# Performance work log

Hardware: AMD Instinct MI355X
Metric: run time of the kernel (lower is better)

Reference implementation:

```python
import jax, jax.numpy as jnp
import numpy as np

B, N, E = 8, 64, 192
D_IN, D_PROJ = 1024, 256
F = 16            # cfg.NGM.GNN_FEAT per layer
SK_TAU = 0.05     # cfg.NGM.SK_TAU
SK_ITERS = 10
BIN_ITERS = 10
NN = N * N


def _project(x, Wp, bp, gamma, beta):
    # self.projection: Linear(1024,256) -> BatchNorm1d(256) (batch stats) -> ReLU
    B_, M, _ = x.shape
    h = x.reshape(B_ * M, -1) @ Wp + bp
    mu = h.mean(0)
    var = h.var(0)
    h = (h - mu) / jnp.sqrt(var + 1e-5) * gamma + beta
    return jax.nn.relu(h).reshape(B_, M, -1)


def _l2n(x):
    return x / jnp.clip(jnp.linalg.norm(x, axis=-1, keepdims=True), 1e-12)


def _log_sinkhorn(log_s, iters):
    for _ in range(iters):
        log_s = log_s - jax.nn.logsumexp(log_s, axis=2, keepdims=True)
        log_s = log_s - jax.nn.logsumexp(log_s, axis=1, keepdims=True)
    return jnp.exp(log_s)


def _build_K(Ke, Kp, s1, d1, s2, d2):
    # construct_sparse_aff_mat: K[a2*N+a1, b2*N+b1] += Ke[e1, e2]
    rows = s2[None, :] * N + s1[:, None]      # [E, E]
    cols = d2[None, :] * N + d1[:, None]      # [E, E]
    flat = (rows.astype(jnp.int32) * NN + cols.astype(jnp.int32)).ravel()
    K = jnp.zeros((NN * NN,), Ke.dtype).at[flat].add(Ke.ravel()).reshape(NN, NN)
    diag = jnp.arange(NN)
    # diagonal holds vec(Kp^T) (ordering a2*N + a1, matching emb = Kp.T.reshape(-1,1))
    return K.at[diag, diag].set(Kp.T.ravel())


def setup_inputs() -> dict:
    key = jax.random.key(0)
    ks = jax.random.split(key, 32)
    inp = {}
    inp['x1'] = jax.random.normal(ks[0], (B, N, D_IN), jnp.float32)
    inp['x2'] = jax.random.normal(ks[1], (B, N, D_IN), jnp.float32)
    inp['e1'] = jax.random.normal(ks[2], (B, E, D_IN), jnp.float32)
    inp['e2'] = jax.random.normal(ks[3], (B, E, D_IN), jnp.float32)
    inp['Wp'] = jax.random.normal(ks[4], (D_IN, D_PROJ), jnp.float32) * 0.02
    inp['bp'] = jnp.zeros((D_PROJ,), jnp.float32)
    inp['gamma'] = jnp.ones((D_PROJ,), jnp.float32)
    inp['beta'] = jnp.zeros((D_PROJ,), jnp.float32)
    in_dims = [1, F + 1, F + 1]
    for i, din in enumerate(in_dims):
        inp[f'W{i}'] = jax.random.normal(ks[5 + 3 * i], (din, F), jnp.float32) * 0.2
        inp[f'b{i}'] = jnp.zeros((F,), jnp.float32)
        inp[f'S{i}'] = jax.random.normal(ks[6 + 3 * i], (F, 1), jnp.float32) * 0.2
        inp[f'c{i}'] = jnp.zeros((1,), jnp.float32)
    inp['Wc'] = jax.random.normal(ks[20], (F + 1, 1), jnp.float32) * 0.2
    inp['bc'] = jnp.zeros((1,), jnp.float32)
    inp['bin_value'] = jnp.ones((1,), jnp.float32) * 0.2
    inp['src1'] = jax.random.randint(ks[21], (B, E), 0, N, jnp.int32)
    inp['dst1'] = jax.random.randint(ks[22], (B, E), 0, N, jnp.int32)
    inp['src2'] = jax.random.randint(ks[23], (B, E), 0, N, jnp.int32)
    inp['dst2'] = jax.random.randint(ks[24], (B, E), 0, N, jnp.int32)
    return inp


def reference(x1, x2, e1, e2, Wp, bp, gamma, beta,
              W0, b0, S0, c0, W1, b1, S1, c1, W2, b2, S2, c2,
              Wc, bc, bin_value, src1, dst1, src2, dst2):
    # unary / quadratic affinities via projected, L2-normalized inner products
    p1 = _project(x1, Wp, bp, gamma, beta)
    p2 = _project(x2, Wp, bp, gamma, beta)
    q1 = _project(e1, Wp, bp, gamma, beta)
    q2 = _project(e2, Wp, bp, gamma, beta)
    Kp = jnp.einsum('bnd,bmd->bnm', _l2n(p1), _l2n(p2))        # [B, N1, N2]
    Ke = 0.5 * jnp.einsum('bed,bfd->bef', _l2n(q1), _l2n(q2))  # [B, E1, E2]
    # sparse Kronecker affinity assembled densely (association graph adjacency)
    K = jax.vmap(_build_K)(Ke, Kp, src1, dst1, src2, dst2)     # [B, NN, NN]
    A = (K > 0).astype(K.dtype)
    deg = jnp.clip(A.sum(-1), 1.0)                              # [B, NN]
    x = Kp.transpose(0, 2, 1).reshape(B, NN, 1)                 # emb = vec(Kp^T)
    for (W, b, S, c) in ((W0, b0, S0, c0), (W1, b1, S1, c1), (W2, b2, S2, c2)):
        msg = jnp.einsum('bij,bjc->bic', K, x) / deg[..., None]  # sparse matvec (memory-bound)
        h = jax.nn.relu(msg @ W + b)                             # [B, NN, F]
        v = (h @ S + c).reshape(B, N, N)                         # row order a2*N+a1 -> [B, N2, N1]
        ss = _log_sinkhorn(v.transpose(0, 2, 1) / SK_TAU, SK_ITERS)  # Sinkhorn embedding channel
        x = jnp.concatenate([h, ss.transpose(0, 2, 1).reshape(B, NN, 1)], -1)
    v = (x @ Wc + bc).reshape(B, N, N)
    s = v.transpose(0, 2, 1)                                    # [B, N1, N2]
    # BinSinkhorn: pad with learned bin value, dual normalization, strip bin
    binv = bin_value[0]
    ls = jnp.concatenate([s, jnp.full((B, 1, N), binv, s.dtype)], 1)
    ls = jnp.concatenate([ls, jnp.full((B, N + 1, 1), binv, s.dtype)], 2)
    P = _log_sinkhorn(ls, BIN_ITERS)
    ss = P[:, :N, :N]
    return ss / jax.lax.stop_gradient(ss.max())
```

## Files before the change

### kernel.cpp

```cpp
#include <hip/hip_runtime.h>

constexpr int kB   = 8;
constexpr int kN   = 64;
constexpr int kE   = 192;
constexpr int kDin = 1024;
constexpr int kDp  = 256;
constexpr int kNN  = 4096;
constexpr float kTauInv = 20.0f;
constexpr int kXS  = 16;
constexpr int kXP  = 18;

typedef float vfloat4 __attribute__((ext_vector_type(4)));

struct SmemGemm {
    float As[2][16][68]; float Ws[2][16][68];
    float colS[64], colS2[64];
};
struct SmemCsr  {
    int km1[4096], km2[4096];
    short es1[kE], es2[kE], rp1[kE], rp2[kE];
    int cnt1[64], cnt2[64], pos1[64], pos2[64];
    int ccnt1[kE], ccnt2[kE], cpos1[kE], cpos2[kE];
};
union __align__(16) SmemK1 { SmemGemm g; SmemCsr csr; };

__global__ __launch_bounds__(256) void k_projcsr(
    const float* __restrict__ x1, const float* __restrict__ x2,
    const float* __restrict__ e1, const float* __restrict__ e2,
    const float* __restrict__ Wp, const float* __restrict__ bp,
    const int* __restrict__ src1, const int* __restrict__ dst1,
    const int* __restrict__ src2, const int* __restrict__ dst2,
    float* __restrict__ hbuf, float* __restrict__ stats,
    int* __restrict__ off1, int* __restrict__ off2,
    int* __restrict__ lst1, int* __restrict__ lst2,
    int* __restrict__ rep1g, int* __restrict__ rep2g,
    int* __restrict__ coff1, int* __restrict__ coff2,
    int* __restrict__ clst1, int* __restrict__ clst2)
{
    const int bid = blockIdx.x, t = threadIdx.x;
    __shared__ SmemK1 u;

    if (bid < 256) {
        const int rt = bid >> 2, ct = bid & 3;
        const int grow0 = rt * 64, col0 = ct * 64;
        const int seg = (rt < 8) ? 0 : (rt < 16 ? 1 : (rt < 40 ? 2 : 3));
        const float* src; int lrow0;
        if (rt < 8)       { src = x1; lrow0 = grow0; }
        else if (rt < 16) { src = x2; lrow0 = grow0 - 512; }
        else if (rt < 40) { src = e1; lrow0 = grow0 - 1024; }
        else              { src = e2; lrow0 = grow0 - 2560; }

        const int tx = t & 15, ty = t >> 4;
        const int arow = t >> 2, acol = (t & 3) * 4;
        const int wrow = t >> 4, wcol = (t & 15) * 4;
        if (t < 64) { u.g.colS[t] = 0.f; u.g.colS2[t] = 0.f; }

        const float* Abase = src + (size_t)(lrow0 + arow) * kDin + acol;
        const float* Wbase = Wp + (size_t)wrow * kDp + col0 + wcol;

        float4 a4 = *(const float4*)Abase;
        float4 w4 = *(const float4*)Wbase;
        float acc[4][4] = {};

        for (int c = 0; c < 64; ++c) {
            const int cur = c & 1;
            u.g.As[cur][acol + 0][arow] = a4.x;
            u.g.As[cur][acol + 1][arow] = a4.y;
            u.g.As[cur][acol + 2][arow] = a4.z;
            u.g.As[cur][acol + 3][arow] = a4.w;
            *(float4*)&u.g.Ws[cur][wrow][wcol] = w4;
            __syncthreads();
            if (c < 63) {
                a4 = *(const float4*)(Abase + (c + 1) * 16);
                w4 = *(const float4*)(Wbase + (size_t)(c + 1) * 16 * kDp);
            }
#pragma unroll
            for (int kk = 0; kk < 16; ++kk) {
                float4 av = *(const float4*)&u.g.As[cur][kk][ty * 4];
                float4 wv = *(const float4*)&u.g.Ws[cur][kk][tx * 4];
                float a[4] = {av.x, av.y, av.z, av.w};
                float w[4] = {wv.x, wv.y, wv.z, wv.w};
#pragma unroll
                for (int i = 0; i < 4; ++i)
#pragma unroll
                    for (int j = 0; j < 4; ++j)
                        acc[i][j] += a[i] * w[j];
            }
        }
        const float4 bb4 = *(const float4*)&bp[col0 + tx * 4];
        float sC[4] = {0.f, 0.f, 0.f, 0.f}, qC[4] = {0.f, 0.f, 0.f, 0.f};
#pragma unroll
        for (int i = 0; i < 4; ++i) {
            const int row = grow0 + ty * 4 + i;
            vfloat4 v;
            v.x = acc[i][0] + bb4.x; v.y = acc[i][1] + bb4.y;
            v.z = acc[i][2] + bb4.z; v.w = acc[i][3] + bb4.w;
            __builtin_nontemporal_store(v, (vfloat4*)&hbuf[(size_t)row * kDp + col0 + tx * 4]);
            sC[0] += v.x; sC[1] += v.y; sC[2] += v.z; sC[3] += v.w;
            qC[0] += v.x * v.x; qC[1] += v.y * v.y;
            qC[2] += v.z * v.z; qC[3] += v.w * v.w;
        }
#pragma unroll
        for (int j = 0; j < 4; ++j) {
            atomicAdd(&u.g.colS[tx * 4 + j], sC[j]);
            atomicAdd(&u.g.colS2[tx * 4 + j], qC[j]);
        }
        __syncthreads();
        if (t < 64) {
            atomicAdd(&stats[seg * 512 + col0 + t], u.g.colS[t]);
            atomicAdd(&stats[seg * 512 + 256 + col0 + t], u.g.colS2[t]);
        }
    } else {
        const int b = bid - 256;
        auto& C = u.csr;
        for (int i = t; i < 4096; i += 256) {
            C.km1[i] = 0x7fffffff; C.km2[i] = 0x7fffffff;
        }
        if (t < 64) { C.cnt1[t] = 0; C.cnt2[t] = 0; }
        for (int i = t; i < kE; i += 256) { C.ccnt1[i] = 0; C.ccnt2[i] = 0; }
        __syncthreads();
        if (t < kE) {
            int v1 = src1[b * kE + t], v2 = src2[b * kE + t];
            C.es1[t] = (short)v1; C.es2[t] = (short)v2;
            atomicAdd(&C.cnt1[v1], 1);
            atomicAdd(&C.cnt2[v2], 1);
            atomicMin(&C.km1[v1 * 64 + dst1[b * kE + t]], t);
            atomicMin(&C.km2[v2 * 64 + dst2[b * kE + t]], t);
        }
        __syncthreads();
        if (t < kE) {
            int r1 = C.km1[C.es1[t] * 64 + dst1[b * kE + t]];
            int r2 = C.km2[C.es2[t] * 64 + dst2[b * kE + t]];
            C.rp1[t] = (short)r1; C.rp2[t] = (short)r2;
            rep1g[b * kE + t] = r1; rep2g[b * kE + t] = r2;
            atomicAdd(&C.ccnt1[r1], 1);
            atomicAdd(&C.ccnt2[r2], 1);
        }
        __syncthreads();
        if (t == 0) {
            int a = 0, c = 0;
            for (int v = 0; v < 64; ++v) { C.pos1[v] = a; a += C.cnt1[v]; C.pos2[v] = c; c += C.cnt2[v]; }
            a = 0; c = 0;
            for (int v = 0; v < kE; ++v) { C.cpos1[v] = a; a += C.ccnt1[v]; C.cpos2[v] = c; c += C.ccnt2[v]; }
        }
        __syncthreads();
        if (t < 64) { off1[b * 65 + t] = C.pos1[t]; off2[b * 65 + t] = C.pos2[t]; }
        if (t == 0) { off1[b * 65 + 64] = kE; off2[b * 65 + 64] = kE; }
        if (t < kE) { coff1[b * 193 + t] = C.cpos1[t]; coff2[b * 193 + t] = C.cpos2[t]; }
        if (t == 0) { coff1[b * 193 + kE] = kE; coff2[b * 193 + kE] = kE; }
        __syncthreads();
        if (t < kE) {
            int p = atomicAdd(&C.pos1[C.es1[t]], 1); lst1[b * kE + p] = t;
            int q = atomicAdd(&C.pos2[C.es2[t]], 1); lst2[b * kE + q] = t;
            int cp = atomicAdd(&C.cpos1[C.rp1[t]], 1); clst1[b * kE + cp] = t;
            int cq = atomicAdd(&C.cpos2[C.rp2[t]], 1); clst2[b * kE + cq] = t;
        }
    }
}

struct __align__(16) SmemSim  {
    float Xs[32][36]; float Ys[32][36];
    float muX[256], isX[256], muY[256], isY[256];
    float ga[256], be[256];
    float scX[32], scY[32];
};

__global__ __launch_bounds__(256) void k_sim(
    const float* __restrict__ hbuf, const float* __restrict__ stats,
    const float* __restrict__ gamma, const float* __restrict__ beta,
    float* __restrict__ Kp, float* __restrict__ Ke)
{
    const int bid = blockIdx.x, t = threadIdx.x;
    __shared__ SmemSim u;

    const int id = bid % 40, b = bid / 40;
    int mt, nt_, ldo, segX, segY, xrow0, yrow0; float* outp; float scale;
    if (id < 4) {
        mt = (id >> 1) * 32; nt_ = (id & 1) * 32; ldo = 64;
        xrow0 = b * 64; yrow0 = 512 + b * 64;
        segX = 0; segY = 1;
        outp = Kp + (size_t)b * 4096; scale = 1.0f;
    } else {
        int e = id - 4;
        mt = (e / 6) * 32; nt_ = (e % 6) * 32; ldo = 192;
        xrow0 = 1024 + b * 192; yrow0 = 2560 + b * 192;
        segX = 2; segY = 3;
        outp = Ke + (size_t)b * 36864; scale = 0.5f;
    }
    {
        const float n = (segX < 2) ? 512.f : 1536.f;
        float mu = stats[segX * 512 + t] / n;
        float var = stats[segX * 512 + 256 + t] / n - mu * mu;
        u.muX[t] = mu; u.isX[t] = rsqrtf(var + 1e-5f);
        mu = stats[segY * 512 + t] / n;
        var = stats[segY * 512 + 256 + t] / n - mu * mu;
        u.muY[t] = mu; u.isY[t] = rsqrtf(var + 1e-5f);
        u.ga[t] = gamma[t]; u.be[t] = beta[t];
    }
    __syncthreads();
    {
        const int ri = t >> 2, lane = t & 3;
        const bool isXr = ri < 32;
        const int grow = isXr ? (xrow0 + mt + ri) : (yrow0 + nt_ + (ri - 32));
        const float* mus = isXr ? u.muX : u.muY;
        const float* iss = isXr ? u.isX : u.isY;
        const float* hr = hbuf + (size_t)grow * kDp;
        float ss = 0.f;
        for (int c4 = 0; c4 < 16; ++c4) {
            int c = lane * 64 + c4 * 4;
            float4 v = *(const float4*)&hr[c];
            float p;
            p = fmaxf((v.x - mus[c+0]) * iss[c+0] * u.ga[c+0] + u.be[c+0], 0.f); ss += p * p;
            p = fmaxf((v.y - mus[c+1]) * iss[c+1] * u.ga[c+1] + u.be[c+1], 0.f); ss += p * p;
            p = fmaxf((v.z - mus[c+2]) * iss[c+2] * u.ga[c+2] + u.be[c+2], 0.f); ss += p * p;
            p = fmaxf((v.w - mus[c+3]) * iss[c+3] * u.ga[c+3] + u.be[c+3], 0.f); ss += p * p;
        }
        ss += __shfl_xor(ss, 1);
        ss += __shfl_xor(ss, 2);
        if (lane == 0) {
            float sc = 1.f / fmaxf(sqrtf(ss), 1e-12f);
            if (isXr) u.scX[ri] = sc; else u.scY[ri - 32] = sc;
        }
    }
    __syncthreads();
    const int row = t >> 3, kq = t & 7;
    const int ty = t >> 4, tx = t & 15;
    const float* Xp = hbuf + (size_t)(xrow0 + mt) * kDp;
    const float* Yp = hbuf + (size_t)(yrow0 + nt_) * kDp;
    float acc[2][2] = {};
    for (int k0 = 0; k0 < kDp; k0 += 32) {
        const int c = k0 + kq * 4;
        float4 xa = *(const float4*)(Xp + (size_t)row * kDp + c);
        float4 ya = *(const float4*)(Yp + (size_t)row * kDp + c);
        const float sx = u.scX[row], sy = u.scY[row];
        u.Xs[kq*4+0][row] = fmaxf((xa.x - u.muX[c+0]) * u.isX[c+0] * u.ga[c+0] + u.be[c+0], 0.f) * sx;
        u.Xs[kq*4+1][row] = fmaxf((xa.y - u.muX[c+1]) * u.isX[c+1] * u.ga[c+1] + u.be[c+1], 0.f) * sx;
        u.Xs[kq*4+2][row] = fmaxf((xa.z - u.muX[c+2]) * u.isX[c+2] * u.ga[c+2] + u.be[c+2], 0.f) * sx;
        u.Xs[kq*4+3][row] = fmaxf((xa.w - u.muX[c+3]) * u.isX[c+3] * u.ga[c+3] + u.be[c+3], 0.f) * sx;
        u.Ys[kq*4+0][row] = fmaxf((ya.x - u.muY[c+0]) * u.isY[c+0] * u.ga[c+0] + u.be[c+0], 0.f) * sy;
        u.Ys[kq*4+1][row] = fmaxf((ya.y - u.muY[c+1]) * u.isY[c+1] * u.ga[c+1] + u.be[c+1], 0.f) * sy;
        u.Ys[kq*4+2][row] = fmaxf((ya.z - u.muY[c+2]) * u.isY[c+2] * u.ga[c+2] + u.be[c+2], 0.f) * sy;
        u.Ys[kq*4+3][row] = fmaxf((ya.w - u.muY[c+3]) * u.isY[c+3] * u.ga[c+3] + u.be[c+3], 0.f) * sy;
        __syncthreads();
#pragma unroll
        for (int kk = 0; kk < 32; ++kk) {
            float2 xv = *(const float2*)&u.Xs[kk][ty * 2];
            float2 yv = *(const float2*)&u.Ys[kk][tx * 2];
            acc[0][0] += xv.x * yv.x; acc[0][1] += xv.x * yv.y;
            acc[1][0] += xv.y * yv.x; acc[1][1] += xv.y * yv.y;
        }
        __syncthreads();
    }
#pragma unroll
    for (int i = 0; i < 2; ++i)
#pragma unroll
        for (int j = 0; j < 2; ++j)
            __builtin_nontemporal_store(scale * acc[i][j],
                &outp[(size_t)(mt + ty * 2 + i) * ldo + nt_ + tx * 2 + j]);
}

struct __align__(16) SmemLayer {
    float mat[64][68]; float fL[64], gL[64];
    float WL[17 * 16]; float bL[16], SL[16]; float c0v;
    float WcL[17];
    int jd2[kE]; int il[kE]; float msgT[64][18];
    int co1L[kE + 1], co2L[kE + 1];
    short cl1L[kE], cl2L[kE];
    float xs[64][kXP];
};

__device__ void sink64_local(int b, int t, float (*mat)[68], float* fL, float* gL,
                             const float* __restrict__ vin)
{
    const float4* v4 = (const float4*)(vin + b * kNN);
    for (int i = t; i < 1024; i += 256) {
        float4 v = v4[i];
        int idx = i * 4;
        int q = idx >> 6, p = idx & 63;
        mat[p][q]     = v.x * kTauInv;
        mat[p + 1][q] = v.y * kTauInv;
        mat[p + 2][q] = v.z * kTauInv;
        mat[p + 3][q] = v.w * kTauInv;
    }
    if (t < 64) { fL[t] = 0.f; gL[t] = 0.f; }
    __syncthreads();
    const int r = t >> 2, s = t & 3;
    float tv[16];
    for (int it = 0; it < 10; ++it) {
        float mx = -1e30f;
#pragma unroll
        for (int k = 0; k < 16; ++k) {
            float v = mat[r][s + 4 * k] + gL[s + 4 * k];
            tv[k] = v; mx = fmaxf(mx, v);
        }
        mx = fmaxf(mx, __shfl_xor(mx, 1));
        mx = fmaxf(mx, __shfl_xor(mx, 2));
        float sum = 0.f;
#pragma unroll
        for (int k = 0; k < 16; ++k) sum += __expf(tv[k] - mx);
        sum += __shfl_xor(sum, 1);
        sum += __shfl_xor(sum, 2);
        if (s == 0) fL[r] = -(mx + __logf(sum));
        __syncthreads();
        mx = -1e30f;
#pragma unroll
        for (int k = 0; k < 16; ++k) {
            float v = mat[s + 4 * k][r] + fL[s + 4 * k];
            tv[k] = v; mx = fmaxf(mx, v);
        }
        mx = fmaxf(mx, __shfl_xor(mx, 1));
        mx = fmaxf(mx, __shfl_xor(mx, 2));
        sum = 0.f;
#pragma unroll
        for (int k = 0; k < 16; ++k) sum += __expf(tv[k] - mx);
        sum += __shfl_xor(sum, 1);
        sum += __shfl_xor(sum, 2);
        if (s == 0) gL[r] = -(mx + __logf(sum));
        __syncthreads();
    }
    const float fr = fL[r];
#pragma unroll
    for (int k = 0; k < 16; ++k) {
        int q = s + 4 * k;
        mat[r][q] = __expf(mat[r][q] + fr + gL[q]);
    }
    __syncthreads();
}

template <int C, bool LASTP>
__device__ void layer_body(int bid, int t, SmemLayer& L,
    const int* __restrict__ off1, const int* __restrict__ lst1,
    const int* __restrict__ off2, const int* __restrict__ lst2,
    const int* __restrict__ d1, const int* __restrict__ d2,
    const int* __restrict__ rep1g, const int* __restrict__ rep2g,
    const int* __restrict__ coff1, const int* __restrict__ coff2,
    const int* __restrict__ clst1, const int* __restrict__ clst2,
    const float* __restrict__ Ke, const float* __restrict__ x,
    const float* __restrict__ Kp, int* __restrict__ degcnt,
    const float* __restrict__ W, const float* __restrict__ bb,
    const float* __restrict__ S, const float* __restrict__ c0,
    const float* __restrict__ Wc,
    const float* __restrict__ vprev, float* __restrict__ xn,
    float* __restrict__ vcbuf, float* __restrict__ vout)
{
    const int r2 = bid & 63, b = bid >> 6;
    for (int k = t; k < C * 16; k += 256) L.WL[k] = W[k];
    if (t < 16) { L.bL[t] = bb[t]; L.SL[t] = S[t]; }
    if (t == 0) L.c0v = c0[0];
    if (LASTP && t < 17) L.WcL[t] = Wc[t];
    const int j0 = off2[b * 65 + r2];
    const int n2 = off2[b * 65 + r2 + 1] - j0;
    for (int k = t; k < n2; k += 256) {
        int j = lst2[b * kE + j0 + k];
        int v = (j << 8) | d2[b * kE + j];
        if (C == 1 && rep2g[b * kE + j] == j) v |= 1 << 16;
        L.jd2[k] = v;
    }
    for (int k = t; k < kE; k += 256) {
        int i = lst1[b * kE + k];
        int v = (i << 8) | d1[b * kE + i];
        if (C == 1 && rep1g[b * kE + i] == i) v |= 1 << 16;
        L.il[k] = v;
    }
    if constexpr (C == 1) {
        for (int k = t; k < kE + 1; k += 256) {
            L.co1L[k] = coff1[b * 193 + k];
            L.co2L[k] = coff2[b * 193 + k];
        }
        for (int k = t; k < kE; k += 256) {
            L.cl1L[k] = (short)clst1[b * kE + k];
            L.cl2L[k] = (short)clst2[b * kE + k];
        }
    }
    if constexpr (C == 17) {
        sink64_local(b, t, L.mat, L.fL, L.gL, vprev);
    } else {
        __syncthreads();
    }

    const int r1 = t >> 2, lane = t & 3;
    const int i0 = off1[b * 65 + r1], i1 = off1[b * 65 + r1 + 1];
    const float* Keb = Ke + (size_t)b * kE * kE;
    const float* KpB = Kp + (size_t)b * kNN;
    int degLocal = 0;

    if constexpr (C == 1) {
        float acc = 0.f;
        for (int k = 0; k < n2; ++k) {
            int pk = L.jd2[k], j = (pk >> 8) & 255, dd2 = pk & 255;
            for (int m = i0 + lane; m < i1; m += 4) {
                int pi = L.il[m], i = (pi >> 8) & 255, dd1 = pi & 255;
                if (dd2 == r2 && dd1 == r1) continue;
                acc += Keb[(size_t)i * kE + j] * KpB[dd1 * 64 + dd2];
            }
        }
        acc += __shfl_xor(acc, 1);
        acc += __shfl_xor(acc, 2);
        if (lane == 0) L.msgT[r1][0] = acc;
        for (int m = i0 + lane; m < i1; m += 4) {
            int pi = L.il[m];
            if (!(pi >> 16)) continue;
            int i = (pi >> 8) & 255, dd1 = pi & 255;
            for (int k = 0; k < n2; ++k) {
                int pk = L.jd2[k];
                if (!(pk >> 16)) continue;
                int j = (pk >> 8) & 255, dd2 = pk & 255;
                float sum = 0.f;
                for (int mm = L.co1L[i]; mm < L.co1L[i + 1]; ++mm) {
                    const float* kr = Keb + (size_t)L.cl1L[mm] * kE;
                    for (int nn = L.co2L[j]; nn < L.co2L[j + 1]; ++nn)
                        sum += kr[L.cl2L[nn]];
                }
                if ((r2 * 64 + r1) != (dd2 * 64 + dd1) && sum > 0.0f) ++degLocal;
            }
        }
        degLocal += __shfl_xor(degLocal, 1);
        degLocal += __shfl_xor(degLocal, 2);
    } else {
        const float* xb = x + (size_t)b * kNN * kXS;
        float acc[5];
#pragma unroll
        for (int cc = 0; cc < 5; ++cc) acc[cc] = 0.f;
        for (int k = 0; k < n2; ++k) {
            int pk = L.jd2[k], j = (pk >> 8) & 255, dd2 = pk & 255;
            __syncthreads();
            {
                const float4* src4 = (const float4*)(xb + (size_t)(dd2 * 64) * kXS);
                float4 vv = src4[t];
                const int row = t >> 2, c4 = (t & 3) * 4;
                L.xs[row][c4 + 0] = vv.x; L.xs[row][c4 + 1] = vv.y;
                L.xs[row][c4 + 2] = vv.z; L.xs[row][c4 + 3] = vv.w;
            }
            __syncthreads();
            for (int m = i0; m < i1; ++m) {
                int pi = L.il[m], dd1 = pi & 255;
                if (dd2 == r2 && dd1 == r1) continue;
                int i = (pi >> 8) & 255;
                float kv = Keb[(size_t)i * kE + j];
                const float* xc = &L.xs[dd1][0];
                acc[0] += kv * xc[lane];
                acc[1] += kv * xc[lane + 4];
                acc[2] += kv * xc[lane + 8];
                acc[3] += kv * xc[lane + 12];
                if (lane == 0) acc[4] += kv * L.mat[dd1][dd2];
            }
        }
#pragma unroll
        for (int cc = 0; cc < 5; ++cc) {
            int c = lane + cc * 4;
            if (c < C) L.msgT[r1][c] = acc[cc];
        }
    }
    __syncthreads();

    const int row = r2 * 64 + r1;
    const int idx = b * kNN + row;
    const float kd = KpB[r1 * 64 + r2];
    int degv;
    if constexpr (C == 1) {
        degv = degLocal;
        if (lane == 0) __builtin_nontemporal_store(degLocal, &degcnt[idx]);
    } else {
        degv = degcnt[idx];
    }
    const float dg = fmaxf((float)(degv + (kd > 0.f ? 1 : 0)), 1.f);
    float m[C];
    if constexpr (C == 1) {
        m[0] = (L.msgT[r1][0] + kd * kd) / dg;
    } else {
        float4 xa  = *(const float4*)(x + (size_t)idx * kXS + 0);
        float4 xb4 = *(const float4*)(x + (size_t)idx * kXS + 4);
        float4 xc4 = *(const float4*)(x + (size_t)idx * kXS + 8);
        float4 xd4 = *(const float4*)(x + (size_t)idx * kXS + 12);
        m[0]  = (L.msgT[r1][0]  + kd * xa.x) / dg;
        m[1]  = (L.msgT[r1][1]  + kd * xa.y) / dg;
        m[2]  = (L.msgT[r1][2]  + kd * xa.z) / dg;
        m[3]  = (L.msgT[r1][3]  + kd * xa.w) / dg;
        m[4]  = (L.msgT[r1][4]  + kd * xb4.x) / dg;
        m[5]  = (L.msgT[r1][5]  + kd * xb4.y) / dg;
        m[6]  = (L.msgT[r1][6]  + kd * xb4.z) / dg;
        m[7]  = (L.msgT[r1][7]  + kd * xb4.w) / dg;
        m[8]  = (L.msgT[r1][8]  + kd * xc4.x) / dg;
        m[9]  = (L.msgT[r1][9]  + kd * xc4.y) / dg;
        m[10] = (L.msgT[r1][10] + kd * xc4.z) / dg;
        m[11] = (L.msgT[r1][11] + kd * xc4.w) / dg;
        m[12] = (L.msgT[r1][12] + kd * xd4.x) / dg;
        m[13] = (L.msgT[r1][13] + kd * xd4.y) / dg;
        m[14] = (L.msgT[r1][14] + kd * xd4.z) / dg;
        m[15] = (L.msgT[r1][15] + kd * xd4.w) / dg;
        m[16] = (L.msgT[r1][16] + kd * L.mat[r1][r2]) / dg;
    }
    float h[4];
    float vpart = 0.f;
#pragma unroll
    for (int ff = 0; ff < 4; ++ff) {
        int f = lane * 4 + ff;
        float a = L.bL[f];
#pragma unroll
        for (int c = 0; c < C; ++c) a += m[c] * L.WL[c * 16 + f];
        h[ff] = fmaxf(a, 0.f);
        vpart += h[ff] * L.SL[f];
    }
    if constexpr (!LASTP) {
        vfloat4 hv; hv.x = h[0]; hv.y = h[1]; hv.z = h[2]; hv.w = h[3];
        __builtin_nontemporal_store(hv, (vfloat4*)(xn + (size_t)idx * kXS + lane * 4));
    } else {
        float vcp = h[0] * L.WcL[lane * 4 + 0] + h[1] * L.WcL[lane * 4 + 1]
                  + h[2] * L.WcL[lane * 4 + 2] + h[3] * L.WcL[lane * 4 + 3];
        vcp += __shfl_xor(vcp, 1);
        vcp += __shfl_xor(vcp, 2);
        if (lane == 0) __builtin_nontemporal_store(vcp, &vcbuf[idx]);
    }
    vpart += __shfl_xor(vpart, 1);
    vpart += __shfl_xor(vpart, 2);
    if (lane == 0) __builtin_nontemporal_store(vpart + L.c0v, &vout[idx]);
}

__global__ __launch_bounds__(256) void k_l0(
    const int* __restrict__ off1, const int* __restrict__ lst1,
    const int* __restrict__ off2, const int* __restrict__ lst2,
    const int* __restrict__ dst1, const int* __restrict__ dst2,
    const int* __restrict__ rep1g, const int* __restrict__ rep2g,
    const int* __restrict__ coff1, const int* __restrict__ coff2,
    const int* __restrict__ clst1, const int* __restrict__ clst2,
    const float* __restrict__ Ke, const float* __restrict__ Kp,
    int* __restrict__ degcnt,
    const float* __restrict__ W0, const float* __restrict__ b0,
    const float* __restrict__ S0, const float* __restrict__ c0,
    float* __restrict__ xA, float* __restrict__ vA)
{
    __shared__ SmemLayer L;
    layer_body<1, false>(blockIdx.x, threadIdx.x, L,
        off1, lst1, off2, lst2, dst1, dst2, rep1g, rep2g,
        coff1, coff2, clst1, clst2, Ke, nullptr, Kp, degcnt,
        W0, b0, S0, c0, nullptr, nullptr, xA, nullptr, vA);
}

__global__ __launch_bounds__(256) void k_l1(
    const int* __restrict__ off1, const int* __restrict__ lst1,
    const int* __restrict__ off2, const int* __restrict__ lst2,
    const int* __restrict__ dst1, const int* __restrict__ dst2,
    const float* __restrict__ Ke, const float* __restrict__ Kp,
    int* __restrict__ degcnt,
    const float* __restrict__ W1, const float* __restrict__ b1,
    const float* __restrict__ S1, const float* __restrict__ c1,
    const float* __restrict__ xA, const float* __restrict__ vA,
    float* __restrict__ xB, float* __restrict__ vB)
{
    __shared__ SmemLayer L;
    layer_body<17, false>(blockIdx.x, threadIdx.x, L,
        off1, lst1, off2, lst2, dst1, dst2, nullptr, nullptr,
        nullptr, nullptr, nullptr, nullptr, Ke, xA, Kp, degcnt,
        W1, b1, S1, c1, nullptr, vA, xB, nullptr, vB);
}

__global__ __launch_bounds__(256) void k_l2(
    const int* __restrict__ off1, const int* __restrict__ lst1,
    const int* __restrict__ off2, const int* __restrict__ lst2,
    const int* __restrict__ dst1, const int* __restrict__ dst2,
    const float* __restrict__ Ke, const float* __restrict__ Kp,
    int* __restrict__ degcnt,
    const float* __restrict__ W2, const float* __restrict__ b2,
    const float* __restrict__ S2, const float* __restrict__ c2,
    const float* __restrict__ Wc,
    const float* __restrict__ xB, const float* __restrict__ vB,
    float* __restrict__ vcbuf, float* __restrict__ vA)
{
    __shared__ SmemLayer L;
    layer_body<17, true>(blockIdx.x, threadIdx.x, L,
        off1, lst1, off2, lst2, dst1, dst2, nullptr, nullptr,
        nullptr, nullptr, nullptr, nullptr, Ke, xB, Kp, degcnt,
        W2, b2, S2, c2, Wc, vB, nullptr, vcbuf, vA);
}

struct __align__(16) SmemSink {
    float mat[65][68]; float fL[65], gL[65];
    float wred[4];
};

__global__ __launch_bounds__(256) void k_final(
    const float* __restrict__ vA, const float* __restrict__ vcbuf,
    const float* __restrict__ Wc, const float* __restrict__ bc,
    const float* __restrict__ binv,
    int* __restrict__ bars, float* __restrict__ out)
{
    const int b = blockIdx.x, t = threadIdx.x;
    __shared__ SmemSink S;

    sink64_local(b, t, S.mat, S.fL, S.gL, vA);

    const float Wc16 = Wc[16], bcv = bc[0], binvv = binv[0];
    const float* vcb = vcbuf + (size_t)b * kNN;
    for (int idx = t; idx < 65 * 65; idx += 256) {
        int q = idx / 65, p = idx - q * 65;
        float v;
        if (p < 64 && q < 64)
            v = vcb[q * 64 + p] + S.mat[p][q] * Wc16 + bcv;
        else v = binvv;
        S.mat[p][q] = v;
    }
    if (t < 65) { S.fL[t] = 0.f; S.gL[t] = 0.f; }
    __syncthreads();

    const int r = t >> 2, s = t & 3;
    for (int it = 0; it < 10; ++it) {
        for (int rr = r; rr < 65; rr += 64) {
            float tv[17];
            float mx = -1e30f;
#pragma unroll
            for (int k = 0; k < 17; ++k) {
                int q = s + 4 * k;
                float v = (q < 65) ? S.mat[rr][q] + S.gL[q] : -1e30f;
                tv[k] = v; mx = fmaxf(mx, v);
            }
            mx = fmaxf(mx, __shfl_xor(mx, 1));
            mx = fmaxf(mx, __shfl_xor(mx, 2));
            float sum = 0.f;
#pragma unroll
            for (int k = 0; k < 17; ++k) sum += __expf(tv[k] - mx);
            sum += __shfl_xor(sum, 1);
            sum += __shfl_xor(sum, 2);
            if (s == 0) S.fL[rr] = -(mx + __logf(sum));
        }
        __syncthreads();
        for (int rr = r; rr < 65; rr += 64) {
            float tv[17];
            float mx = -1e30f;
#pragma unroll
            for (int k = 0; k < 17; ++k) {
                int p = s + 4 * k;
                float v = (p < 65) ? S.mat[p][rr] + S.fL[p] : -1e30f;
                tv[k] = v; mx = fmaxf(mx, v);
            }
            mx = fmaxf(mx, __shfl_xor(mx, 1));
            mx = fmaxf(mx, __shfl_xor(mx, 2));
            float sum = 0.f;
#pragma unroll
            for (int k = 0; k < 17; ++k) sum += __expf(tv[k] - mx);
            sum += __shfl_xor(sum, 1);
            sum += __shfl_xor(sum, 2);
            if (s == 0) S.gL[rr] = -(mx + __logf(sum));
        }
        __syncthreads();
    }

    float ev[16];
    float lmax = 0.f;
    {
        const float fr = S.fL[r];
#pragma unroll
        for (int k = 0; k < 16; ++k) {
            int q = s + 4 * k;
            ev[k] = __expf(S.mat[r][q] + fr + S.gL[q]);
            lmax = fmaxf(lmax, ev[k]);
        }
    }
#pragma unroll
    for (int o = 32; o >= 1; o >>= 1) lmax = fmaxf(lmax, __shfl_xor(lmax, o));
    if ((t & 63) == 0) S.wred[t >> 6] = lmax;
    __syncthreads();
    int* mcnt = bars + 3584;
    int* gmax = bars + 3600;
    if (t == 0) {
        float mb = fmaxf(fmaxf(S.wred[0], S.wred[1]), fmaxf(S.wred[2], S.wred[3]));
        atomicMax(gmax, __float_as_int(mb));
        asm volatile("s_waitcnt vmcnt(0)" ::: "memory");
        __hip_atomic_fetch_add(mcnt, 1, __ATOMIC_RELAXED, __HIP_MEMORY_SCOPE_AGENT);
        while (__hip_atomic_load(mcnt, __ATOMIC_RELAXED, __HIP_MEMORY_SCOPE_AGENT) < 8)
            __builtin_amdgcn_s_sleep(2);
    }
    __syncthreads();
    const float inv = 1.f / __int_as_float(
        __hip_atomic_load(gmax, __ATOMIC_RELAXED, __HIP_MEMORY_SCOPE_AGENT));
#pragma unroll
    for (int k = 0; k < 16; ++k) {
        int q = s + 4 * k;
        out[((size_t)b * kN + r) * kN + q] = ev[k] * inv;
    }
}

extern "C" void kernel_launch(void* const* d_in, const int* in_sizes, int n_in,
                              void* d_out, int out_size, void* d_ws, size_t ws_size,
                              hipStream_t stream)
{
    (void)in_sizes; (void)n_in; (void)out_size; (void)ws_size;

    const float* x1    = (const float*)d_in[0];
    const float* x2    = (const float*)d_in[1];
    const float* e1    = (const float*)d_in[2];
    const float* e2    = (const float*)d_in[3];
    const float* Wp    = (const float*)d_in[4];
    const float* bp    = (const float*)d_in[5];
    const float* gamma = (const float*)d_in[6];
    const float* beta  = (const float*)d_in[7];
    const float* W0 = (const float*)d_in[8];
    const float* b0 = (const float*)d_in[9];
    const float* S0 = (const float*)d_in[10];
    const float* c0 = (const float*)d_in[11];
    const float* W1 = (const float*)d_in[12];
    const float* b1 = (const float*)d_in[13];
    const float* S1 = (const float*)d_in[14];
    const float* c1 = (const float*)d_in[15];
    const float* W2 = (const float*)d_in[16];
    const float* b2 = (const float*)d_in[17];
    const float* S2 = (const float*)d_in[18];
    const float* c2 = (const float*)d_in[19];
    const float* Wc = (const float*)d_in[20];
    const float* bc = (const float*)d_in[21];
    const float* binv = (const float*)d_in[22];
    const int* src1 = (const int*)d_in[23];
    const int* dst1 = (const int*)d_in[24];
    const int* src2 = (const int*)d_in[25];
    const int* dst2 = (const int*)d_in[26];

    float* out = (float*)d_out;
    float* wsf = (float*)d_ws;

    float* hbuf  = wsf;
    float* Kp    = hbuf + 1048576;
    float* Ke    = Kp + 32768;
    float* vA    = Ke + 294912;
    float* vB    = vA + 32768;
    float* xA    = vB + 32768;
    float* xB    = xA + 524288;
    float* vcbuf = xB + 524288;
    int*   degcnt = (int*)(vcbuf + 32768);
    int*   off1 = degcnt + 32768;
    int*   off2 = off1 + 520;
    int*   lst1 = off2 + 520;
    int*   lst2 = lst1 + 1536;
    int*   rep1g = lst2 + 1536;
    int*   rep2g = rep1g + 1536;
    int*   coff1 = rep2g + 1536;
    int*   coff2 = coff1 + 1544;
    int*   clst1 = coff2 + 1544;
    int*   clst2 = clst1 + 1536;
    float* stats = (float*)(clst2 + 1536);
    int*   bars  = (int*)(stats + 2048);

    (void)hipMemsetAsync(stats, 0, (2048 + 4096) * sizeof(int), stream);
    k_projcsr<<<dim3(264), dim3(256), 0, stream>>>(
        x1, x2, e1, e2, Wp, bp, src1, dst1, src2, dst2, hbuf, stats,
        off1, off2, lst1, lst2, rep1g, rep2g, coff1, coff2, clst1, clst2);
    k_sim<<<dim3(320), dim3(256), 0, stream>>>(hbuf, stats, gamma, beta, Kp, Ke);
    k_l0<<<dim3(512), dim3(256), 0, stream>>>(
        off1, lst1, off2, lst2, dst1, dst2, rep1g, rep2g,
        coff1, coff2, clst1, clst2, Ke, Kp, degcnt,
        W0, b0, S0, c0, xA, vA);
    k_l1<<<dim3(512), dim3(256), 0, stream>>>(
        off1, lst1, off2, lst2, dst1, dst2, Ke, Kp, degcnt,
        W1, b1, S1, c1, xA, vA, xB, vB);
    k_l2<<<dim3(512), dim3(256), 0, stream>>>(
        off1, lst1, off2, lst2, dst1, dst2, Ke, Kp, degcnt,
        W2, b2, S2, c2, Wc, xB, vB, vcbuf, vA);
    k_final<<<dim3(8), dim3(256), 0, stream>>>(vA, vcbuf, Wc, bc, binv, bars, out);
}
```

Before: 323.5 us.

## Split-K projection GEMM with separate reduce kernel; widen final Sinkhorn block

The projection GEMM is split along K into two halves. This doubles the number of blocks from 256 to 512 for better CU occupancy, and writes partial sums to a new workspace buffer. A new reduce kernel adds the partials and the bias, writes hbuf and accumulates the BatchNorm column statistics. The final kernel now runs with 576 threads and 8 lanes per row. It keeps row and column values in registers across the Sinkhorn iterations and inlines the layer-2 Sinkhorn instead of calling the shared helper. The trade-off is an extra launch, 8 MB of extra partial-sum traffic, and removal of the shared-memory pre-reduction of the stats atomics.

```diff
diff --git a/kernel.cpp b/kernel.cpp
--- a/kernel.cpp
+++ b/kernel.cpp
@@ -12,10 +12,7 @@
 
 typedef float vfloat4 __attribute__((ext_vector_type(4)));
 
-struct SmemGemm {
-    float As[2][16][68]; float Ws[2][16][68];
-    float colS[64], colS2[64];
-};
+struct SmemGemm { float As[2][16][68]; float Ws[2][16][68]; };
 struct SmemCsr  {
     int km1[4096], km2[4096];
     short es1[kE], es2[kE], rp1[kE], rp2[kE];
@@ -27,10 +24,10 @@
 __global__ __launch_bounds__(256) void k_projcsr(
     const float* __restrict__ x1, const float* __restrict__ x2,
     const float* __restrict__ e1, const float* __restrict__ e2,
-    const float* __restrict__ Wp, const float* __restrict__ bp,
+    const float* __restrict__ Wp,
     const int* __restrict__ src1, const int* __restrict__ dst1,
     const int* __restrict__ src2, const int* __restrict__ dst2,
-    float* __restrict__ hbuf, float* __restrict__ stats,
+    float* __restrict__ P,
     int* __restrict__ off1, int* __restrict__ off2,
     int* __restrict__ lst1, int* __restrict__ lst2,
     int* __restrict__ rep1g, int* __restrict__ rep2g,
@@ -40,10 +37,10 @@
     const int bid = blockIdx.x, t = threadIdx.x;
     __shared__ SmemK1 u;
 
-    if (bid < 256) {
-        const int rt = bid >> 2, ct = bid & 3;
+    if (bid < 512) {
+        const int z = bid >> 8;
+        const int rt = (bid >> 2) & 63, ct = bid & 3;
         const int grow0 = rt * 64, col0 = ct * 64;
-        const int seg = (rt < 8) ? 0 : (rt < 16 ? 1 : (rt < 40 ? 2 : 3));
         const float* src; int lrow0;
         if (rt < 8)       { src = x1; lrow0 = grow0; }
         else if (rt < 16) { src = x2; lrow0 = grow0 - 512; }
@@ -53,16 +50,15 @@
         const int tx = t & 15, ty = t >> 4;
         const int arow = t >> 2, acol = (t & 3) * 4;
         const int wrow = t >> 4, wcol = (t & 15) * 4;
-        if (t < 64) { u.g.colS[t] = 0.f; u.g.colS2[t] = 0.f; }
-
-        const float* Abase = src + (size_t)(lrow0 + arow) * kDin + acol;
-        const float* Wbase = Wp + (size_t)wrow * kDp + col0 + wcol;
+
+        const float* Abase = src + (size_t)(lrow0 + arow) * kDin + z * 512 + acol;
+        const float* Wbase = Wp + (size_t)(z * 512 + wrow) * kDp + col0 + wcol;
 
         float4 a4 = *(const float4*)Abase;
         float4 w4 = *(const float4*)Wbase;
         float acc[4][4] = {};
 
-        for (int c = 0; c < 64; ++c) {
+        for (int c = 0; c < 32; ++c) {
             const int cur = c & 1;
             u.g.As[cur][acol + 0][arow] = a4.x;
             u.g.As[cur][acol + 1][arow] = a4.y;
@@ -70,7 +66,7 @@
             u.g.As[cur][acol + 3][arow] = a4.w;
             *(float4*)&u.g.Ws[cur][wrow][wcol] = w4;
             __syncthreads();
-            if (c < 63) {
+            if (c < 31) {
                 a4 = *(const float4*)(Abase + (c + 1) * 16);
                 w4 = *(const float4*)(Wbase + (size_t)(c + 1) * 16 * kDp);
             }
@@ -87,31 +83,16 @@
                         acc[i][j] += a[i] * w[j];
             }
         }
-        const float4 bb4 = *(const float4*)&bp[col0 + tx * 4];
-        float sC[4] = {0.f, 0.f, 0.f, 0.f}, qC[4] = {0.f, 0.f, 0.f, 0.f};
+        float* Pz = P + (size_t)z * 1048576;
 #pragma unroll
         for (int i = 0; i < 4; ++i) {
             const int row = grow0 + ty * 4 + i;
             vfloat4 v;
-            v.x = acc[i][0] + bb4.x; v.y = acc[i][1] + bb4.y;
-            v.z = acc[i][2] + bb4.z; v.w = acc[i][3] + bb4.w;
-            __builtin_nontemporal_store(v, (vfloat4*)&hbuf[(size_t)row * kDp + col0 + tx * 4]);
-            sC[0] += v.x; sC[1] += v.y; sC[2] += v.z; sC[3] += v.w;
-            qC[0] += v.x * v.x; qC[1] += v.y * v.y;
-            qC[2] += v.z * v.z; qC[3] += v.w * v.w;
-        }
-#pragma unroll
-        for (int j = 0; j < 4; ++j) {
-            atomicAdd(&u.g.colS[tx * 4 + j], sC[j]);
-            atomicAdd(&u.g.colS2[tx * 4 + j], qC[j]);
-        }
-        __syncthreads();
-        if (t < 64) {
-            atomicAdd(&stats[seg * 512 + col0 + t], u.g.colS[t]);
-            atomicAdd(&stats[seg * 512 + 256 + col0 + t], u.g.colS2[t]);
+            v.x = acc[i][0]; v.y = acc[i][1]; v.z = acc[i][2]; v.w = acc[i][3];
+            __builtin_nontemporal_store(v, (vfloat4*)&Pz[(size_t)row * kDp + col0 + tx * 4]);
         }
     } else {
-        const int b = bid - 256;
+        const int b = bid - 512;
         auto& C = u.csr;
         for (int i = t; i < 4096; i += 256) {
             C.km1[i] = 0x7fffffff; C.km2[i] = 0x7fffffff;
@@ -156,6 +137,26 @@
             int cq = atomicAdd(&C.cpos2[C.rp2[t]], 1); clst2[b * kE + cq] = t;
         }
     }
+}
+
+__global__ __launch_bounds__(256) void k_reduce(
+    const float* __restrict__ P, const float* __restrict__ bp,
+    float* __restrict__ hbuf, float* __restrict__ stats)
+{
+    const int t = threadIdx.x;
+    const int r0 = blockIdx.x * 16;
+    const int seg = (r0 < 512) ? 0 : (r0 < 1024 ? 1 : (r0 < 2560 ? 2 : 3));
+    const float bb = bp[t];
+    float s = 0.f, s2 = 0.f;
+#pragma unroll
+    for (int rr = 0; rr < 16; ++rr) {
+        size_t o = (size_t)(r0 + rr) * kDp + t;
+        float v = P[o] + P[o + 1048576] + bb;
+        hbuf[o] = v;
+        s += v; s2 += v * v;
+    }
+    atomicAdd(&stats[seg * 512 + t], s);
+    atomicAdd(&stats[seg * 512 + 256 + t], s2);
 }
 
 struct __align__(16) SmemSim  {
@@ -573,86 +574,137 @@
         W2, b2, S2, c2, Wc, vB, nullptr, vcbuf, vA);
 }
 
-struct __align__(16) SmemSink {
+struct __align__(16) SmemSinkF {
     float mat[65][68]; float fL[65], gL[65];
-    float wred[4];
+    float wred[9];
 };
 
-__global__ __launch_bounds__(256) void k_final(
+__global__ __launch_bounds__(576) void k_final(
     const float* __restrict__ vA, const float* __restrict__ vcbuf,
     const float* __restrict__ Wc, const float* __restrict__ bc,
     const float* __restrict__ binv,
     int* __restrict__ bars, float* __restrict__ out)
 {
     const int b = blockIdx.x, t = threadIdx.x;
-    __shared__ SmemSink S;
-
-    sink64_local(b, t, S.mat, S.fL, S.gL, vA);
-
-    const float Wc16 = Wc[16], bcv = bc[0], binvv = binv[0];
-    const float* vcb = vcbuf + (size_t)b * kNN;
-    for (int idx = t; idx < 65 * 65; idx += 256) {
-        int q = idx / 65, p = idx - q * 65;
-        float v;
-        if (p < 64 && q < 64)
-            v = vcb[q * 64 + p] + S.mat[p][q] * Wc16 + bcv;
-        else v = binvv;
-        S.mat[p][q] = v;
+    __shared__ SmemSinkF S;
+
+    for (int i = t; i < kNN; i += 576) {
+        int q = i >> 6, p = i & 63;
+        S.mat[p][q] = vA[b * kNN + i] * kTauInv;
     }
     if (t < 65) { S.fL[t] = 0.f; S.gL[t] = 0.f; }
     __syncthreads();
 
-    const int r = t >> 2, s = t & 3;
-    for (int it = 0; it < 10; ++it) {
-        for (int rr = r; rr < 65; rr += 64) {
-            float tv[17];
+    const int r = t >> 3, s = t & 7;
+
+    {
+        const bool act = r < 64;
+        const int cnt = act ? ((64 - s + 7) >> 3) : 0;
+        float Lr[8], Lc[8];
+        for (int k = 0; k < cnt; ++k) {
+            Lr[k] = S.mat[r][s + 8 * k];
+            Lc[k] = S.mat[s + 8 * k][r];
+        }
+        __syncthreads();
+        float tv[8];
+        for (int it = 0; it < 10; ++it) {
             float mx = -1e30f;
-#pragma unroll
-            for (int k = 0; k < 17; ++k) {
-                int q = s + 4 * k;
-                float v = (q < 65) ? S.mat[rr][q] + S.gL[q] : -1e30f;
-                tv[k] = v; mx = fmaxf(mx, v);
-            }
+            for (int k = 0; k < cnt; ++k) { tv[k] = Lr[k] + S.gL[s + 8 * k]; mx = fmaxf(mx, tv[k]); }
             mx = fmaxf(mx, __shfl_xor(mx, 1));
             mx = fmaxf(mx, __shfl_xor(mx, 2));
+            mx = fmaxf(mx, __shfl_xor(mx, 4));
             float sum = 0.f;
-#pragma unroll
-            for (int k = 0; k < 17; ++k) sum += __expf(tv[k] - mx);
+            for (int k = 0; k < cnt; ++k) sum += __expf(tv[k] - mx);
             sum += __shfl_xor(sum, 1);
             sum += __shfl_xor(sum, 2);
-            if (s == 0) S.fL[rr] = -(mx + __logf(sum));
-        }
-        __syncthreads();
-        for (int rr = r; rr < 65; rr += 64) {
-            float tv[17];
-            float mx = -1e30f;
-#pragma unroll
-            for (int k = 0; k < 17; ++k) {
-                int p = s + 4 * k;
-                float v = (p < 65) ? S.mat[p][rr] + S.fL[p] : -1e30f;
-                tv[k] = v; mx = fmaxf(mx, v);
-            }
+            sum += __shfl_xor(sum, 4);
+            if (act && s == 0) S.fL[r] = -(mx + __logf(sum));
+            __syncthreads();
+            mx = -1e30f;
+            for (int k = 0; k < cnt; ++k) { tv[k] = Lc[k] + S.fL[s + 8 * k]; mx = fmaxf(mx, tv[k]); }
             mx = fmaxf(mx, __shfl_xor(mx, 1));
             mx = fmaxf(mx, __shfl_xor(mx, 2));
-            float sum = 0.f;
-#pragma unroll
-            for (int k = 0; k < 17; ++k) sum += __expf(tv[k] - mx);
+            mx = fmaxf(mx, __shfl_xor(mx, 4));
+            sum = 0.f;
+            for (int k = 0; k < cnt; ++k) sum += __expf(tv[k] - mx);
             sum += __shfl_xor(sum, 1);
             sum += __shfl_xor(sum, 2);
-            if (s == 0) S.gL[rr] = -(mx + __logf(sum));
-        }
-        __syncthreads();
-    }
-
-    float ev[16];
+            sum += __shfl_xor(sum, 4);
+            if (act && s == 0) S.gL[r] = -(mx + __logf(sum));
+            __syncthreads();
+        }
+        if (act) {
+            const float fr = S.fL[r];
+            for (int k = 0; k < cnt; ++k) {
+                int q = s + 8 * k;
+                S.mat[r][q] = __expf(Lr[k] + fr + S.gL[q]);
+            }
+        }
+    }
+    __syncthreads();
+
+    {
+        const float Wc16 = Wc[16], bcv = bc[0], binvv = binv[0];
+        const float* vcb = vcbuf + (size_t)b * kNN;
+        for (int idx = t; idx < 65 * 65; idx += 576) {
+            int q = idx / 65, p = idx - q * 65;
+            float v;
+            if (p < 64 && q < 64)
+                v = vcb[q * 64 + p] + S.mat[p][q] * Wc16 + bcv;
+            else v = binvv;
+            S.mat[p][q] = v;
+        }
+        if (t < 65) { S.fL[t] = 0.f; S.gL[t] = 0.f; }
+    }
+    __syncthreads();
+
+    const bool act = r < 65;
+    const int cnt = act ? ((65 - s + 7) >> 3) : 0;
+    float Lrow[9], Lcol[9];
+    for (int k = 0; k < cnt; ++k) {
+        Lrow[k] = S.mat[r][s + 8 * k];
+        Lcol[k] = S.mat[s + 8 * k][r];
+    }
+    __syncthreads();
+
+    float tv[9];
+    for (int it = 0; it < 10; ++it) {
+        float mx = -1e30f;
+        for (int k = 0; k < cnt; ++k) { tv[k] = Lrow[k] + S.gL[s + 8 * k]; mx = fmaxf(mx, tv[k]); }
+        mx = fmaxf(mx, __shfl_xor(mx, 1));
+        mx = fmaxf(mx, __shfl_xor(mx, 2));
+        mx = fmaxf(mx, __shfl_xor(mx, 4));
+        float sum = 0.f;
+        for (int k = 0; k < cnt; ++k) sum += __expf(tv[k] - mx);
+        sum += __shfl_xor(sum, 1);
+        sum += __shfl_xor(sum, 2);
+        sum += __shfl_xor(sum, 4);
+        if (act && s == 0) S.fL[r] = -(mx + __logf(sum));
+        __syncthreads();
+        mx = -1e30f;
+        for (int k = 0; k < cnt; ++k) { tv[k] = Lcol[k] + S.fL[s + 8 * k]; mx = fmaxf(mx, tv[k]); }
+        mx = fmaxf(mx, __shfl_xor(mx, 1));
+        mx = fmaxf(mx, __shfl_xor(mx, 2));
+        mx = fmaxf(mx, __shfl_xor(mx, 4));
+        sum = 0.f;
+        for (int k = 0; k < cnt; ++k) sum += __expf(tv[k] - mx);
+        sum += __shfl_xor(sum, 1);
+        sum += __shfl_xor(sum, 2);
+        sum += __shfl_xor(sum, 4);
+        if (act && s == 0) S.gL[r] = -(mx + __logf(sum));
+        __syncthreads();
+    }
+
+    float ev[9];
     float lmax = 0.f;
-    {
+    if (act && r < 64) {
         const float fr = S.fL[r];
-#pragma unroll
-        for (int k = 0; k < 16; ++k) {
-            int q = s + 4 * k;
-            ev[k] = __expf(S.mat[r][q] + fr + S.gL[q]);
-            lmax = fmaxf(lmax, ev[k]);
+        for (int k = 0; k < cnt; ++k) {
+            int q = s + 8 * k;
+            if (q < 64) {
+                ev[k] = __expf(Lrow[k] + fr + S.gL[q]);
+                lmax = fmaxf(lmax, ev[k]);
+            } else ev[k] = 0.f;
         }
     }
 #pragma unroll
@@ -662,7 +714,9 @@
     int* mcnt = bars + 3584;
     int* gmax = bars + 3600;
     if (t == 0) {
-        float mb = fmaxf(fmaxf(S.wred[0], S.wred[1]), fmaxf(S.wred[2], S.wred[3]));
+        float mb = S.wred[0];
+#pragma unroll
+        for (int w = 1; w < 9; ++w) mb = fmaxf(mb, S.wred[w]);
         atomicMax(gmax, __float_as_int(mb));
         asm volatile("s_waitcnt vmcnt(0)" ::: "memory");
         __hip_atomic_fetch_add(mcnt, 1, __ATOMIC_RELAXED, __HIP_MEMORY_SCOPE_AGENT);
@@ -672,10 +726,11 @@
     __syncthreads();
     const float inv = 1.f / __int_as_float(
         __hip_atomic_load(gmax, __ATOMIC_RELAXED, __HIP_MEMORY_SCOPE_AGENT));
-#pragma unroll
-    for (int k = 0; k < 16; ++k) {
-        int q = s + 4 * k;
-        out[((size_t)b * kN + r) * kN + q] = ev[k] * inv;
+    if (act && r < 64) {
+        for (int k = 0; k < cnt; ++k) {
+            int q = s + 8 * k;
+            if (q < 64) out[((size_t)b * kN + r) * kN + q] = ev[k] * inv;
+        }
     }
 }
 
@@ -717,7 +772,8 @@
     float* wsf = (float*)d_ws;
 
     float* hbuf  = wsf;
-    float* Kp    = hbuf + 1048576;
+    float* P     = hbuf + 1048576;
+    float* Kp    = P + 2097152;
     float* Ke    = Kp + 32768;
     float* vA    = Ke + 294912;
     float* vB    = vA + 32768;
@@ -739,9 +795,10 @@
     int*   bars  = (int*)(stats + 2048);
 
     (void)hipMemsetAsync(stats, 0, (2048 + 4096) * sizeof(int), stream);
-    k_projcsr<<<dim3(264), dim3(256), 0, stream>>>(
-        x1, x2, e1, e2, Wp, bp, src1, dst1, src2, dst2, hbuf, stats,
+    k_projcsr<<<dim3(520), dim3(256), 0, stream>>>(
+        x1, x2, e1, e2, Wp, src1, dst1, src2, dst2, P,
         off1, off2, lst1, lst2, rep1g, rep2g, coff1, coff2, clst1, clst2);
+    k_reduce<<<dim3(256), dim3(256), 0, stream>>>(P, bp, hbuf, stats);
     k_sim<<<dim3(320), dim3(256), 0, stream>>>(hbuf, stats, gamma, beta, Kp, Ke);
     k_l0<<<dim3(512), dim3(256), 0, stream>>>(
         off1, lst1, off2, lst2, dst1, dst2, rep1g, rep2g,
@@ -753,5 +810,5 @@
     k_l2<<<dim3(512), dim3(256), 0, stream>>>(
         off1, lst1, off2, lst2, dst1, dst2, Ke, Kp, degcnt,
         W2, b2, S2, c2, Wc, xB, vB, vcbuf, vA);
-    k_final<<<dim3(8), dim3(256), 0, stream>>>(vA, vcbuf, Wc, bc, binv, bars, out);
-}
+    k_final<<<dim3(8), dim3(576), 0, stream>>>(vA, vcbuf, Wc, bc, binv, bars, out);
+}
```

New measurement: 336.1 us. 1.04x slower.
